# Optimization experiments

Measured on AMD Instinct MI355X. Metric: run time of the kernel, lower is better.

Reference implementation:

```python
import jax, jax.numpy as jnp
import numpy as np

C, A, K, S = 128, 64, 24, 4           # molecules, atoms, neighbors, species
RCR, RCA = 5.2, 3.5                   # radial / angular cutoffs (Angstrom)
ETA_R, ETA_A, ZETA = 16.0, 8.0, 32.0
LAYERS = [384, 160, 128, 96, 1]       # per-element MLP
NPAIR = S * (S + 1) // 2              # 10 unordered species pairs

_triu = np.zeros((S, S), np.int32)
_c = 0
for _i in range(S):
    for _j in range(_i, S):
        _triu[_i, _j] = _triu[_j, _i] = _c
        _c += 1
TRIU = jnp.asarray(_triu)
JJ, KK = np.triu_indices(K, 1)        # static pair-of-neighbors indices, T = K(K-1)/2


def setup_inputs() -> dict:
    key = jax.random.key(0)
    ks = jax.random.split(key, 12)
    element_idxs = jax.random.randint(ks[0], (C, A), 0, S, dtype=jnp.int32)
    neighbor_idxs = jax.random.randint(ks[1], (C, A, K), 0, A, dtype=jnp.int32)
    distances = jax.random.uniform(ks[2], (C, A, K), minval=0.8, maxval=5.0, dtype=jnp.float32)
    dirs = jax.random.normal(ks[3], (C, A, K, 3), dtype=jnp.float32)
    dirs = dirs / jnp.linalg.norm(dirs, axis=-1, keepdims=True)
    diff_vectors = dirs * distances[..., None]
    inp = {"element_idxs": element_idxs, "neighbor_idxs": neighbor_idxs,
           "distances": distances, "diff_vectors": diff_vectors}
    k = 4
    for i, (fin, fout) in enumerate(zip(LAYERS[:-1], LAYERS[1:]), 1):
        inp[f"W{i}"] = jax.random.normal(ks[k], (S, fin, fout), dtype=jnp.float32) / np.sqrt(fin).astype(np.float32); k += 1
        inp[f"b{i}"] = jax.random.normal(ks[k], (S, fout), dtype=jnp.float32) * 0.01; k += 1
    return inp


def _fc(d, rc):
    # smooth cosine cutoff, exactly zero beyond rc
    return jnp.where(d < rc, 0.5 * jnp.cos(np.float32(np.pi) * d / rc) + 0.5, 0.0)


def _celu(x, a=0.1):
    return jnp.where(x > 0, x, a * jnp.expm1(x / a))


def reference(element_idxs, neighbor_idxs, distances, diff_vectors,
              W1, b1, W2, b2, W3, b3, W4, b4):
    shfr = jnp.linspace(0.9, RCR, 17, dtype=jnp.float32)[:-1]                 # (16,)
    shfa = jnp.linspace(0.9, RCA, 5, dtype=jnp.float32)[:-1]                  # (4,)
    shfz = (jnp.arange(8, dtype=jnp.float32) + 0.5) * np.float32(np.pi / 8)   # (8,)

    # species of each neighbor: (C,A,K)
    nspec = element_idxs[jnp.arange(C)[:, None, None], neighbor_idxs]

    # ---- radial sub-AEV: (C,A,S,16) ----
    fcr = _fc(distances, RCR)
    rterm = 0.25 * jnp.exp(-ETA_R * (distances[..., None] - shfr) ** 2) * fcr[..., None]  # (C,A,K,16)
    oh_s = jax.nn.one_hot(nspec, S, dtype=rterm.dtype)                                     # (C,A,K,S)
    radial = jnp.einsum('cakr,caks->casr', rterm, oh_s).reshape(C, A, S * 16)

    # ---- angular sub-AEV over neighbor pairs (j<k): T = K(K-1)/2 ----
    d1, d2 = distances[..., JJ], distances[..., KK]                 # (C,A,T)
    v1, v2 = diff_vectors[..., JJ, :], diff_vectors[..., KK, :]      # (C,A,T,3)
    cosang = jnp.sum(v1 * v2, axis=-1) / (d1 * d2)
    ang = jnp.arccos(0.95 * cosang)                                  # torchani's 0.95 nan-guard
    f1 = ((1.0 + jnp.cos(ang[..., None] - shfz)) * 0.5) ** ZETA      # (C,A,T,8)
    f2 = jnp.exp(-ETA_A * ((d1 + d2) * 0.5)[..., None] - shfa * 0.0) if False else \
         jnp.exp(-ETA_A * (((d1 + d2) * 0.5)[..., None] - shfa) ** 2)  # (C,A,T,4)
    fc12 = _fc(d1, RCA) * _fc(d2, RCA)                               # (C,A,T)
    aterm = (2.0 * f1[..., :, None] * f2[..., None, :] * fc12[..., None, None]).reshape(C, A, JJ.size, 32)
    pidx = TRIU[nspec[..., JJ], nspec[..., KK]]                      # (C,A,T) in [0,10)
    oh_p = jax.nn.one_hot(pidx, NPAIR, dtype=aterm.dtype)            # (C,A,T,10)
    angular = jnp.einsum('catf,catp->capf', aterm, oh_p).reshape(C, A, NPAIR * 32)

    aev = jnp.concatenate([radial, angular], axis=-1)                # (C,A,384)

    # ---- per-element MLPs (computed for all species, then gathered) ----
    h = _celu(jnp.einsum('caf,sfo->caso', aev, W1) + b1)
    h = _celu(jnp.einsum('casf,sfo->caso', h, W2) + b2)
    h = _celu(jnp.einsum('casf,sfo->caso', h, W3) + b3)
    out = (jnp.einsum('casf,sfo->caso', h, W4) + b4)[..., 0]         # (C,A,S)
    atomic = jnp.take_along_axis(out, element_idxs[..., None], axis=2)[..., 0]  # (C,A)
    return atomic.sum(axis=-1)                                       # (C,) molecular energies
```

## Files before the change

kernel.cpp:

```cpp
#include <hip/hip_runtime.h>
#include <math.h>

constexpr int C_ = 128, A_ = 64, K_ = 24, S_ = 4;
constexpr int NATOM = C_ * A_;
constexpr int FAEV = 384;
constexpr float RCR = 5.2f, RCA = 3.5f;
constexpr float PI_F = 3.14159265358979323846f;
constexpr float K_A2 = -8.0f  * 1.44269504f;
constexpr float K_R2 = -64.0f * 1.44269504f;
constexpr float SQRT095 = 0.974679434f;
constexpr float SQRT2   = 1.41421356237f;

constexpr int MLP_TILES = 288;

__global__ __launch_bounds__(256) void aev_kernel(const int* __restrict__ element_idxs,
                                                  const int* __restrict__ neighbor_idxs,
                                                  const float* __restrict__ distances,
                                                  const float* __restrict__ diff_vectors,
                                                  float* __restrict__ aev_out,
                                                  int* __restrict__ mol_cnt,
                                                  int* __restrict__ mol_lst,
                                                  float* __restrict__ out) {
    const int blk = blockIdx.x;
    const int c   = blk >> 4;
    const int t   = threadIdx.x;

    __shared__ int    elem_s[A_];
    __shared__ float4 u4_s[4][K_];
    __shared__ float  fcr_s[4][K_];
    __shared__ float  fca_s[4][K_];
    __shared__ int    spec_s[4][K_];
    __shared__ int    bidx_s[4][S_][K_];
    __shared__ int    nsp_s[4][S_];

    if (t < A_) elem_s[t] = element_idxs[c * A_ + t];
    __syncthreads();

    if ((blk & 15) == 0) {
        if (t < S_) {
            int n = 0;
            int* lst = mol_lst + (c * S_ + t) * A_;
            for (int a = 0; a < A_; ++a)
                if (elem_s[a] == t) lst[n++] = a;
            mol_cnt[c * S_ + t] = n;
        } else if (t == S_) {
            out[c] = 0.0f;
        }
    }

    if (t < 4 * K_) {
        int m = t / K_, k = t - m * K_;
        int base = (blk * 4 + m) * K_ + k;
        int nb = neighbor_idxs[base];
        float d = distances[base];
        float inv = __builtin_amdgcn_rcpf(d) * SQRT095;
        float4 u;
        u.x = diff_vectors[base * 3 + 0] * inv;
        u.y = diff_vectors[base * 3 + 1] * inv;
        u.z = diff_vectors[base * 3 + 2] * inv;
        u.w = 0.5f * d;
        u4_s[m][k] = u;
        spec_s[m][k] = elem_s[nb];
        fcr_s[m][k] = (d < RCR) ? (0.5f * __cosf(PI_F * d * (1.0f / RCR)) + 0.5f) : 0.0f;
        fca_s[m][k] = (d < RCA) ? (SQRT2 * (0.5f * __cosf(PI_F * d * (1.0f / RCA)) + 0.5f)) : 0.0f;
    }
    __syncthreads();

    if (t < 4 * S_) {
        int m = t >> 2, sp = t & 3, n = 0;
        #pragma unroll
        for (int k = 0; k < K_; ++k)
            if (fca_s[m][k] > 0.0f && spec_s[m][k] == sp) bidx_s[m][sp][n++] = k;
        nsp_s[m][sp] = n;
    }
    __syncthreads();

    const int m      = t >> 6;
    const int lane   = t & 63;
    const int lane32 = lane & 31;
    const int par    = lane >> 5;
    float* aev = aev_out + (size_t)(blk * 4 + m) * FAEV;

    {
        const int   spg   = lane >> 4;
        const float shfrh = 0.5f * (0.9f + 0.26875f * (float)(lane & 15));
        float acc = 0.0f;
        #pragma unroll
        for (int k = 0; k < K_; ++k) {
            float hd = u4_s[m][k].w;
            float df = hd - shfrh;
            float term = 0.25f * exp2f(df * df * K_R2) * fcr_s[m][k];
            if (spec_s[m][k] == spg) acc += term;
        }
        aev[lane] = acc;
    }

    const int zz = lane32 >> 2, yy = lane32 & 3;
    const float cz2 = 0.5f * __cosf(((float)zz + 0.5f) * (PI_F / 8.0f));
    const float sz2 = 0.5f * __sinf(((float)zz + 0.5f) * (PI_F / 8.0f));
    const float shfa_l = 0.9f + 0.65f * (float)yy;

    auto pair_term = [&](int j, int k2) -> float {
        float4 u1 = u4_s[m][j], u2 = u4_s[m][k2];
        float ca = u1.x * u2.x + u1.y * u2.y + u1.z * u2.z;
        float sa = sqrtf(1.0f - ca * ca);
        float dd = (u1.w + u2.w) - shfa_l;
        float f2 = exp2f(dd * dd * K_A2);
        float x  = 0.5f + ca * cz2 + sa * sz2;
        float x2 = x * x, x4 = x2 * x2, x8 = x4 * x4, x16 = x8 * x8;
        float tc = fca_s[m][j] * fca_s[m][k2];
        return (x16 * x16) * (f2 * tc);
    };

    #pragma unroll
    for (int spa = 0; spa < 4; ++spa) {
        #pragma unroll
        for (int spb = spa; spb < 4; ++spb) {
            const int pidx = spa * (9 - spa) / 2 + (spb - spa);
            const int na  = nsp_s[m][spa];
            const int nb2 = nsp_s[m][spb];
            float acc = 0.0f;
            if (spa == spb) {
                int jj = 0, kk = 1 + par;
                while (jj < na - 1 && kk >= na) { int ov = kk - na; ++jj; kk = jj + 1 + ov; }
                while (jj < na - 1) {
                    acc += pair_term(bidx_s[m][spa][jj], bidx_s[m][spa][kk]);
                    kk += 2;
                    while (jj < na - 1 && kk >= na) { int ov = kk - na; ++jj; kk = jj + 1 + ov; }
                }
            } else {
                int jj = 0, kk = par;
                while (jj < na && kk >= nb2) { kk -= nb2; ++jj; }
                while (jj < na) {
                    acc += pair_term(bidx_s[m][spa][jj], bidx_s[m][spb][kk]);
                    kk += 2;
                    while (jj < na && kk >= nb2) { kk -= nb2; ++jj; }
                }
            }
            float other = __shfl(acc, lane32 + 32);
            if (lane < 32) aev[64 + pidx * 32 + lane32] = acc + other;
        }
    }
}

__global__ __launch_bounds__(256) void mlp_kernel(const float* __restrict__ aev_ws,
                                                  const int* __restrict__ mol_cnt,
                                                  const int* __restrict__ mol_lst,
                                                  const float* __restrict__ W1, const float* __restrict__ b1,
                                                  const float* __restrict__ W2, const float* __restrict__ b2,
                                                  const float* __restrict__ W3, const float* __restrict__ b3,
                                                  const float* __restrict__ W4, const float* __restrict__ b4,
                                                  float* __restrict__ out) {
    const int blk   = blockIdx.x;
    const int s     = blk & 3;
    const int tile0 = blk >> 2;
    const int t     = threadIdx.x;
    const int lane  = t & 63;

    const int c0 = lane * 2, c1 = c0 + 1;
    const int n0 = mol_cnt[c0 * S_ + s];
    const int n1 = mol_cnt[c1 * S_ + s];
    const int pairc = n0 + n1;
    int scan = pairc;
    #pragma unroll
    for (int off = 1; off < 64; off <<= 1) {
        int v = __shfl_up(scan, off);
        if (lane >= off) scan += v;
    }
    const int cntS = __shfl(scan, 63);

    __shared__ __attribute__((aligned(16))) float aev_s[8][FAEV];
    __shared__ __attribute__((aligned(16))) float h1_s[8][160];
    float (*h2_s)[128] = (float(*)[128])&aev_s[0][0];
    float (*h3_s)[96]  = (float(*)[96])(&aev_s[0][0] + 8 * 128);

    const float* W1s = W1 + s * (FAEV * 160);
    const float* b1s = b1 + s * 160;
    const float* W2s = W2 + s * (160 * 128);
    const float* b2s = b2 + s * 128;
    const float* W3s = W3 + s * (128 * 96);
    const float* b3s = b3 + s * 96;
    const float* W4s = W4 + s * 96;
    const float  bb4 = b4[s];

    for (int tile = tile0; tile * 8 < cntS; tile += MLP_TILES) {
        const int base = tile * 8;

        int myAtom = -1;
        #pragma unroll
        for (int m = 0; m < 8; ++m) {
            int g = base + m;
            int atomAbs = -1;
            if (g < cntS) {
                unsigned long long mask = __ballot(scan > g);
                int L = (int)__builtin_ctzll(mask);
                int exclL = __shfl(scan, L) - __shfl(pairc, L);
                int n0L   = __shfl(n0, L);
                int loc = g - exclL;
                int cL  = 2 * L;
                if (loc >= n0L) { cL += 1; loc -= n0L; }
                atomAbs = cL * A_ + mol_lst[(cL * S_ + s) * A_ + loc];
            }
            if ((t >> 5) == m) myAtom = atomAbs;
        }

        {
            int mrow = t >> 5, l = t & 31;
            float4* dst = (float4*)&aev_s[mrow][0];
            if (myAtom >= 0) {
                const float4* src = (const float4*)(aev_ws + (size_t)myAtom * FAEV);
                dst[l]      = src[l];
                dst[l + 32] = src[l + 32];
                dst[l + 64] = src[l + 64];
            } else {
                dst[l]      = make_float4(0.f, 0.f, 0.f, 0.f);
                dst[l + 32] = make_float4(0.f, 0.f, 0.f, 0.f);
                dst[l + 64] = make_float4(0.f, 0.f, 0.f, 0.f);
            }
        }
        __syncthreads();

        if (t < 160) {
            const float* Wp = W1s + t;
            float acc[8];
            #pragma unroll
            for (int m = 0; m < 8; ++m) acc[m] = 0.0f;
            float wa[4], wb[4];
            #pragma unroll
            for (int j = 0; j < 4; ++j) wa[j] = Wp[j * 160];
            for (int f = 0; f < FAEV; f += 8) {
                const int fb = f + 4;
                #pragma unroll
                for (int j = 0; j < 4; ++j) wb[j] = Wp[(fb + j) * 160];
                #pragma unroll
                for (int m = 0; m < 8; ++m) {
                    float4 av = *(const float4*)&aev_s[m][f];
                    acc[m] += av.x * wa[0] + av.y * wa[1] + av.z * wa[2] + av.w * wa[3];
                }
                const int fa = (f + 8 < FAEV) ? f + 8 : 0;
                #pragma unroll
                for (int j = 0; j < 4; ++j) wa[j] = Wp[(fa + j) * 160];
                #pragma unroll
                for (int m = 0; m < 8; ++m) {
                    float4 av = *(const float4*)&aev_s[m][fb];
                    acc[m] += av.x * wb[0] + av.y * wb[1] + av.z * wb[2] + av.w * wb[3];
                }
            }
            float bb = b1s[t];
            #pragma unroll
            for (int m = 0; m < 8; ++m) {
                float x = acc[m] + bb;
                h1_s[m][t] = (x > 0.f) ? x : 0.1f * (__expf(10.f * x) - 1.f);
            }
        }
        __syncthreads();

        if (t < 128) {
            const float* Wp = W2s + t;
            float acc[8];
            #pragma unroll
            for (int m = 0; m < 8; ++m) acc[m] = 0.0f;
            float wa[4], wb[4];
            #pragma unroll
            for (int j = 0; j < 4; ++j) wa[j] = Wp[j * 128];
            for (int f = 0; f < 160; f += 8) {
                const int fb = f + 4;
                #pragma unroll
                for (int j = 0; j < 4; ++j) wb[j] = Wp[(fb + j) * 128];
                #pragma unroll
                for (int m = 0; m < 8; ++m) {
                    float4 av = *(const float4*)&h1_s[m][f];
                    acc[m] += av.x * wa[0] + av.y * wa[1] + av.z * wa[2] + av.w * wa[3];
                }
                const int fa = (f + 8 < 160) ? f + 8 : 0;
                #pragma unroll
                for (int j = 0; j < 4; ++j) wa[j] = Wp[(fa + j) * 128];
                #pragma unroll
                for (int m = 0; m < 8; ++m) {
                    float4 av = *(const float4*)&h1_s[m][fb];
                    acc[m] += av.x * wb[0] + av.y * wb[1] + av.z * wb[2] + av.w * wb[3];
                }
            }
            float bb = b2s[t];
            #pragma unroll
            for (int m = 0; m < 8; ++m) {
                float x = acc[m] + bb;
                h2_s[m][t] = (x > 0.f) ? x : 0.1f * (__expf(10.f * x) - 1.f);
            }
        }
        __syncthreads();

        if (t < 96) {
            const float* Wp = W3s + t;
            float acc[8];
            #pragma unroll
            for (int m = 0; m < 8; ++m) acc[m] = 0.0f;
            float wa[4], wb[4];
            #pragma unroll
            for (int j = 0; j < 4; ++j) wa[j] = Wp[j * 96];
            for (int f = 0; f < 128; f += 8) {
                const int fb = f + 4;
                #pragma unroll
                for (int j = 0; j < 4; ++j) wb[j] = Wp[(fb + j) * 96];
                #pragma unroll
                for (int m = 0; m < 8; ++m) {
                    float4 av = *(const float4*)&h2_s[m][f];
                    acc[m] += av.x * wa[0] + av.y * wa[1] + av.z * wa[2] + av.w * wa[3];
                }
                const int fa = (f + 8 < 128) ? f + 8 : 0;
                #pragma unroll
                for (int j = 0; j < 4; ++j) wa[j] = Wp[(fa + j) * 96];
                #pragma unroll
                for (int m = 0; m < 8; ++m) {
                    float4 av = *(const float4*)&h2_s[m][fb];
                    acc[m] += av.x * wb[0] + av.y * wb[1] + av.z * wb[2] + av.w * wb[3];
                }
            }
            float bb = b3s[t];
            #pragma unroll
            for (int m = 0; m < 8; ++m) {
                float x = acc[m] + bb;
                h3_s[m][t] = (x > 0.f) ? x : 0.1f * (__expf(10.f * x) - 1.f);
            }
        }
        __syncthreads();

        {
            int m = t >> 5, l = t & 31;
            if (myAtom >= 0) {
                float p = h3_s[m][l]      * W4s[l]
                        + h3_s[m][l + 32] * W4s[l + 32]
                        + h3_s[m][l + 64] * W4s[l + 64];
                #pragma unroll
                for (int off = 16; off >= 1; off >>= 1)
                    p += __shfl_xor(p, off, 32);
                if (l == 0) atomicAdd(&out[myAtom >> 6], p + bb4);
            }
        }
        __syncthreads();
    }
}

extern "C" void kernel_launch(void* const* d_in, const int* in_sizes, int n_in,
                              void* d_out, int out_size, void* d_ws, size_t ws_size,
                              hipStream_t stream) {
    const int*   element_idxs  = (const int*)d_in[0];
    const int*   neighbor_idxs = (const int*)d_in[1];
    const float* distances     = (const float*)d_in[2];
    const float* diff_vectors  = (const float*)d_in[3];
    const float* W1 = (const float*)d_in[4];
    const float* b1 = (const float*)d_in[5];
    const float* W2 = (const float*)d_in[6];
    const float* b2 = (const float*)d_in[7];
    const float* W3 = (const float*)d_in[8];
    const float* b3 = (const float*)d_in[9];
    const float* W4 = (const float*)d_in[10];
    const float* b4 = (const float*)d_in[11];
    float* out = (float*)d_out;

    float* aev_ws  = (float*)d_ws;
    int*   mol_cnt = (int*)((char*)d_ws + (size_t)NATOM * FAEV * 4);
    int*   mol_lst = mol_cnt + C_ * S_;

    hipLaunchKernelGGL(aev_kernel, dim3(NATOM / 4), dim3(256), 0, stream,
                       element_idxs, neighbor_idxs, distances, diff_vectors,
                       aev_ws, mol_cnt, mol_lst, out);
    hipLaunchKernelGGL(mlp_kernel, dim3(S_ * MLP_TILES), dim3(256), 0, stream,
                       aev_ws, mol_cnt, mol_lst,
                       W1, b1, W2, b2, W3, b3, W4, b4, out);
}
```

Baseline: 251.7 us.

## Fuse AEV computation into per-species MLP kernel with global species atom lists

New measurement: 273.7 us. +8.7%, slower.

```diff
diff --git a/kernel.cpp b/kernel.cpp
--- a/kernel.cpp
+++ b/kernel.cpp
@@ -11,164 +11,60 @@
 constexpr float SQRT095 = 0.974679434f;
 constexpr float SQRT2   = 1.41421356237f;
 
-constexpr int MLP_TILES = 288;
-
-__global__ __launch_bounds__(256) void aev_kernel(const int* __restrict__ element_idxs,
-                                                  const int* __restrict__ neighbor_idxs,
-                                                  const float* __restrict__ distances,
-                                                  const float* __restrict__ diff_vectors,
-                                                  float* __restrict__ aev_out,
-                                                  int* __restrict__ mol_cnt,
-                                                  int* __restrict__ mol_lst,
-                                                  float* __restrict__ out) {
-    const int blk = blockIdx.x;
-    const int c   = blk >> 4;
-    const int t   = threadIdx.x;
-
-    __shared__ int    elem_s[A_];
-    __shared__ float4 u4_s[4][K_];
-    __shared__ float  fcr_s[4][K_];
-    __shared__ float  fca_s[4][K_];
-    __shared__ int    spec_s[4][K_];
-    __shared__ int    bidx_s[4][S_][K_];
-    __shared__ int    nsp_s[4][S_];
-
-    if (t < A_) elem_s[t] = element_idxs[c * A_ + t];
+__global__ __launch_bounds__(1024) void setup_kernel(const int* __restrict__ elem,
+                                                     int* __restrict__ cnt,
+                                                     int* __restrict__ glist,
+                                                     float* __restrict__ out) {
+    __shared__ int cnt_s[S_];
+    const int t = threadIdx.x;
+    const int lane = t & 63;
+    if (t < S_) cnt_s[t] = 0;
+    if (t < C_) out[t] = 0.0f;
     __syncthreads();
-
-    if ((blk & 15) == 0) {
-        if (t < S_) {
-            int n = 0;
-            int* lst = mol_lst + (c * S_ + t) * A_;
-            for (int a = 0; a < A_; ++a)
-                if (elem_s[a] == t) lst[n++] = a;
-            mol_cnt[c * S_ + t] = n;
-        } else if (t == S_) {
-            out[c] = 0.0f;
-        }
-    }
-
-    if (t < 4 * K_) {
-        int m = t / K_, k = t - m * K_;
-        int base = (blk * 4 + m) * K_ + k;
-        int nb = neighbor_idxs[base];
-        float d = distances[base];
-        float inv = __builtin_amdgcn_rcpf(d) * SQRT095;
-        float4 u;
-        u.x = diff_vectors[base * 3 + 0] * inv;
-        u.y = diff_vectors[base * 3 + 1] * inv;
-        u.z = diff_vectors[base * 3 + 2] * inv;
-        u.w = 0.5f * d;
-        u4_s[m][k] = u;
-        spec_s[m][k] = elem_s[nb];
-        fcr_s[m][k] = (d < RCR) ? (0.5f * __cosf(PI_F * d * (1.0f / RCR)) + 0.5f) : 0.0f;
-        fca_s[m][k] = (d < RCA) ? (SQRT2 * (0.5f * __cosf(PI_F * d * (1.0f / RCA)) + 0.5f)) : 0.0f;
+    for (int a = t; a < NATOM; a += 1024) {
+        int sp = elem[a];
+        unsigned long long lt = (lane == 0) ? 0ULL : ((~0ULL) >> (64 - lane));
+        int pos = 0;
+        #pragma unroll
+        for (int q = 0; q < S_; ++q) {
+            unsigned long long m = __ballot(sp == q);
+            int cw = (int)__popcll(m);
+            int b = 0;
+            if (lane == 0 && cw) b = atomicAdd(&cnt_s[q], cw);
+            b = __shfl(b, 0);
+            if (sp == q) pos = b + (int)__popcll(m & lt);
+        }
+        glist[sp * NATOM + pos] = a;
     }
     __syncthreads();
-
-    if (t < 4 * S_) {
-        int m = t >> 2, sp = t & 3, n = 0;
-        #pragma unroll
-        for (int k = 0; k < K_; ++k)
-            if (fca_s[m][k] > 0.0f && spec_s[m][k] == sp) bidx_s[m][sp][n++] = k;
-        nsp_s[m][sp] = n;
-    }
-    __syncthreads();
-
-    const int m      = t >> 6;
-    const int lane   = t & 63;
-    const int lane32 = lane & 31;
-    const int par    = lane >> 5;
-    float* aev = aev_out + (size_t)(blk * 4 + m) * FAEV;
-
-    {
-        const int   spg   = lane >> 4;
-        const float shfrh = 0.5f * (0.9f + 0.26875f * (float)(lane & 15));
-        float acc = 0.0f;
-        #pragma unroll
-        for (int k = 0; k < K_; ++k) {
-            float hd = u4_s[m][k].w;
-            float df = hd - shfrh;
-            float term = 0.25f * exp2f(df * df * K_R2) * fcr_s[m][k];
-            if (spec_s[m][k] == spg) acc += term;
-        }
-        aev[lane] = acc;
-    }
-
-    const int zz = lane32 >> 2, yy = lane32 & 3;
-    const float cz2 = 0.5f * __cosf(((float)zz + 0.5f) * (PI_F / 8.0f));
-    const float sz2 = 0.5f * __sinf(((float)zz + 0.5f) * (PI_F / 8.0f));
-    const float shfa_l = 0.9f + 0.65f * (float)yy;
-
-    auto pair_term = [&](int j, int k2) -> float {
-        float4 u1 = u4_s[m][j], u2 = u4_s[m][k2];
-        float ca = u1.x * u2.x + u1.y * u2.y + u1.z * u2.z;
-        float sa = sqrtf(1.0f - ca * ca);
-        float dd = (u1.w + u2.w) - shfa_l;
-        float f2 = exp2f(dd * dd * K_A2);
-        float x  = 0.5f + ca * cz2 + sa * sz2;
-        float x2 = x * x, x4 = x2 * x2, x8 = x4 * x4, x16 = x8 * x8;
-        float tc = fca_s[m][j] * fca_s[m][k2];
-        return (x16 * x16) * (f2 * tc);
-    };
-
-    #pragma unroll
-    for (int spa = 0; spa < 4; ++spa) {
-        #pragma unroll
-        for (int spb = spa; spb < 4; ++spb) {
-            const int pidx = spa * (9 - spa) / 2 + (spb - spa);
-            const int na  = nsp_s[m][spa];
-            const int nb2 = nsp_s[m][spb];
-            float acc = 0.0f;
-            if (spa == spb) {
-                int jj = 0, kk = 1 + par;
-                while (jj < na - 1 && kk >= na) { int ov = kk - na; ++jj; kk = jj + 1 + ov; }
-                while (jj < na - 1) {
-                    acc += pair_term(bidx_s[m][spa][jj], bidx_s[m][spa][kk]);
-                    kk += 2;
-                    while (jj < na - 1 && kk >= na) { int ov = kk - na; ++jj; kk = jj + 1 + ov; }
-                }
-            } else {
-                int jj = 0, kk = par;
-                while (jj < na && kk >= nb2) { kk -= nb2; ++jj; }
-                while (jj < na) {
-                    acc += pair_term(bidx_s[m][spa][jj], bidx_s[m][spb][kk]);
-                    kk += 2;
-                    while (jj < na && kk >= nb2) { kk -= nb2; ++jj; }
-                }
-            }
-            float other = __shfl(acc, lane32 + 32);
-            if (lane < 32) aev[64 + pidx * 32 + lane32] = acc + other;
-        }
-    }
+    if (t < S_) cnt[t] = cnt_s[t];
 }
 
-__global__ __launch_bounds__(256) void mlp_kernel(const float* __restrict__ aev_ws,
-                                                  const int* __restrict__ mol_cnt,
-                                                  const int* __restrict__ mol_lst,
-                                                  const float* __restrict__ W1, const float* __restrict__ b1,
-                                                  const float* __restrict__ W2, const float* __restrict__ b2,
-                                                  const float* __restrict__ W3, const float* __restrict__ b3,
-                                                  const float* __restrict__ W4, const float* __restrict__ b4,
-                                                  float* __restrict__ out) {
-    const int blk   = blockIdx.x;
-    const int s     = blk & 3;
-    const int tile0 = blk >> 2;
+__global__ __launch_bounds__(512, 8) void fused_kernel(const int* __restrict__ elem,
+                                                       const int* __restrict__ nbr,
+                                                       const float* __restrict__ dist,
+                                                       const float* __restrict__ dv,
+                                                       const int* __restrict__ cnt,
+                                                       const int* __restrict__ glist,
+                                                       const float* __restrict__ W1, const float* __restrict__ b1,
+                                                       const float* __restrict__ W2, const float* __restrict__ b2,
+                                                       const float* __restrict__ W3, const float* __restrict__ b3,
+                                                       const float* __restrict__ W4, const float* __restrict__ b4,
+                                                       float* __restrict__ out) {
+    const int s     = blockIdx.x >> 8;
+    const int tile0 = blockIdx.x & 255;
     const int t     = threadIdx.x;
+    const int w     = t >> 6;
     const int lane  = t & 63;
-
-    const int c0 = lane * 2, c1 = c0 + 1;
-    const int n0 = mol_cnt[c0 * S_ + s];
-    const int n1 = mol_cnt[c1 * S_ + s];
-    const int pairc = n0 + n1;
-    int scan = pairc;
-    #pragma unroll
-    for (int off = 1; off < 64; off <<= 1) {
-        int v = __shfl_up(scan, off);
-        if (lane >= off) scan += v;
-    }
-    const int cntS = __shfl(scan, 63);
-
+    const int cntS  = cnt[s];
+
+    __shared__ float4        u4_s[8][K_];
+    __shared__ float         fcr_s[8][K_];
+    __shared__ float         fca_s[8][K_];
+    __shared__ int           spec_s[8][K_];
+    __shared__ unsigned char bidx_s[8][S_][K_];
+    __shared__ int           nsp_s[8][S_];
+    __shared__ int           atom_sh[8];
     __shared__ __attribute__((aligned(16))) float aev_s[8][FAEV];
     __shared__ __attribute__((aligned(16))) float h1_s[8][160];
     float (*h2_s)[128] = (float(*)[128])&aev_s[0][0];
@@ -183,48 +79,109 @@
     const float* W4s = W4 + s * 96;
     const float  bb4 = b4[s];
 
-    for (int tile = tile0; tile * 8 < cntS; tile += MLP_TILES) {
-        const int base = tile * 8;
-
-        int myAtom = -1;
-        #pragma unroll
-        for (int m = 0; m < 8; ++m) {
-            int g = base + m;
-            int atomAbs = -1;
-            if (g < cntS) {
-                unsigned long long mask = __ballot(scan > g);
-                int L = (int)__builtin_ctzll(mask);
-                int exclL = __shfl(scan, L) - __shfl(pairc, L);
-                int n0L   = __shfl(n0, L);
-                int loc = g - exclL;
-                int cL  = 2 * L;
-                if (loc >= n0L) { cL += 1; loc -= n0L; }
-                atomAbs = cL * A_ + mol_lst[(cL * S_ + s) * A_ + loc];
-            }
-            if ((t >> 5) == m) myAtom = atomAbs;
-        }
-
-        {
-            int mrow = t >> 5, l = t & 31;
-            float4* dst = (float4*)&aev_s[mrow][0];
-            if (myAtom >= 0) {
-                const float4* src = (const float4*)(aev_ws + (size_t)myAtom * FAEV);
-                dst[l]      = src[l];
-                dst[l + 32] = src[l + 32];
-                dst[l + 64] = src[l + 64];
-            } else {
-                dst[l]      = make_float4(0.f, 0.f, 0.f, 0.f);
-                dst[l + 32] = make_float4(0.f, 0.f, 0.f, 0.f);
-                dst[l + 64] = make_float4(0.f, 0.f, 0.f, 0.f);
-            }
-        }
-        __syncthreads();
-
-        if (t < 160) {
-            const float* Wp = W1s + t;
-            float acc[8];
-            #pragma unroll
-            for (int m = 0; m < 8; ++m) acc[m] = 0.0f;
+    const int lane32 = lane & 31;
+    const int par    = lane >> 5;
+    const int zz = lane32 >> 2, yy = lane32 & 3;
+    const float cz2 = 0.5f * __cosf(((float)zz + 0.5f) * (PI_F / 8.0f));
+    const float sz2 = 0.5f * __sinf(((float)zz + 0.5f) * (PI_F / 8.0f));
+    const float shfa_l = 0.9f + 0.65f * (float)yy;
+
+    for (int tile = tile0; tile * 8 < cntS; tile += 256) {
+        const int g = tile * 8 + w;
+        const int atomAbs = (g < cntS) ? glist[s * NATOM + g] : -1;
+        if (lane == 0) atom_sh[w] = atomAbs;
+
+        if (atomAbs >= 0 && lane < K_) {
+            int base = atomAbs * K_ + lane;
+            int c    = atomAbs >> 6;
+            int nb   = nbr[base];
+            float d  = dist[base];
+            float inv = __builtin_amdgcn_rcpf(d) * SQRT095;
+            float4 u;
+            u.x = dv[base * 3 + 0] * inv;
+            u.y = dv[base * 3 + 1] * inv;
+            u.z = dv[base * 3 + 2] * inv;
+            u.w = 0.5f * d;
+            u4_s[w][lane]  = u;
+            spec_s[w][lane] = elem[(c << 6) + nb];
+            fcr_s[w][lane] = (d < RCR) ? (0.5f * __cosf(PI_F * d * (1.0f / RCR)) + 0.5f) : 0.0f;
+            fca_s[w][lane] = (d < RCA) ? (SQRT2 * (0.5f * __cosf(PI_F * d * (1.0f / RCA)) + 0.5f)) : 0.0f;
+        }
+        __syncthreads();
+
+        if (atomAbs >= 0 && lane < S_) {
+            int n = 0;
+            #pragma unroll
+            for (int k = 0; k < K_; ++k)
+                if (fca_s[w][k] > 0.0f && spec_s[w][k] == lane)
+                    bidx_s[w][lane][n++] = (unsigned char)k;
+            nsp_s[w][lane] = n;
+        }
+        __syncthreads();
+
+        if (atomAbs >= 0) {
+            {
+                const int   spg   = lane >> 4;
+                const float shfrh = 0.5f * (0.9f + 0.26875f * (float)(lane & 15));
+                float acc = 0.0f;
+                #pragma unroll
+                for (int k = 0; k < K_; ++k) {
+                    float hd = u4_s[w][k].w;
+                    float df = hd - shfrh;
+                    float term = 0.25f * exp2f(df * df * K_R2) * fcr_s[w][k];
+                    if (spec_s[w][k] == spg) acc += term;
+                }
+                aev_s[w][lane] = acc;
+            }
+            auto pair_term = [&](int j, int k2) -> float {
+                float4 u1 = u4_s[w][j], u2 = u4_s[w][k2];
+                float ca = u1.x * u2.x + u1.y * u2.y + u1.z * u2.z;
+                float sa = sqrtf(1.0f - ca * ca);
+                float dd = (u1.w + u2.w) - shfa_l;
+                float f2 = exp2f(dd * dd * K_A2);
+                float x  = 0.5f + ca * cz2 + sa * sz2;
+                float x2 = x * x, x4 = x2 * x2, x8 = x4 * x4, x16 = x8 * x8;
+                float tc = fca_s[w][j] * fca_s[w][k2];
+                return (x16 * x16) * (f2 * tc);
+            };
+            #pragma unroll
+            for (int spa = 0; spa < 4; ++spa) {
+                #pragma unroll
+                for (int spb = spa; spb < 4; ++spb) {
+                    const int pidx = spa * (9 - spa) / 2 + (spb - spa);
+                    const int na  = nsp_s[w][spa];
+                    const int nb2 = nsp_s[w][spb];
+                    float acc = 0.0f;
+                    if (spa == spb) {
+                        int jj = 0, kk = 1 + par;
+                        while (jj < na - 1 && kk >= na) { int ov = kk - na; ++jj; kk = jj + 1 + ov; }
+                        while (jj < na - 1) {
+                            acc += pair_term((int)bidx_s[w][spa][jj], (int)bidx_s[w][spa][kk]);
+                            kk += 2;
+                            while (jj < na - 1 && kk >= na) { int ov = kk - na; ++jj; kk = jj + 1 + ov; }
+                        }
+                    } else {
+                        int jj = 0, kk = par;
+                        while (jj < na && kk >= nb2) { kk -= nb2; ++jj; }
+                        while (jj < na) {
+                            acc += pair_term((int)bidx_s[w][spa][jj], (int)bidx_s[w][spb][kk]);
+                            kk += 2;
+                            while (jj < na && kk >= nb2) { kk -= nb2; ++jj; }
+                        }
+                    }
+                    float other = __shfl(acc, lane32 + 32);
+                    if (lane < 32) aev_s[w][64 + pidx * 32 + lane32] = acc + other;
+                }
+            }
+        }
+        __syncthreads();
+
+        if (t < 320) {
+            const int h  = (t >= 160) ? 1 : 0;
+            const int o  = t - h * 160;
+            const int mb = h * 4;
+            const float* Wp = W1s + o;
+            float acc[4] = {0.f, 0.f, 0.f, 0.f};
             float wa[4], wb[4];
             #pragma unroll
             for (int j = 0; j < 4; ++j) wa[j] = Wp[j * 160];
@@ -233,33 +190,34 @@
                 #pragma unroll
                 for (int j = 0; j < 4; ++j) wb[j] = Wp[(fb + j) * 160];
                 #pragma unroll
-                for (int m = 0; m < 8; ++m) {
-                    float4 av = *(const float4*)&aev_s[m][f];
+                for (int m = 0; m < 4; ++m) {
+                    float4 av = *(const float4*)&aev_s[mb + m][f];
                     acc[m] += av.x * wa[0] + av.y * wa[1] + av.z * wa[2] + av.w * wa[3];
                 }
                 const int fa = (f + 8 < FAEV) ? f + 8 : 0;
                 #pragma unroll
                 for (int j = 0; j < 4; ++j) wa[j] = Wp[(fa + j) * 160];
                 #pragma unroll
-                for (int m = 0; m < 8; ++m) {
-                    float4 av = *(const float4*)&aev_s[m][fb];
+                for (int m = 0; m < 4; ++m) {
+                    float4 av = *(const float4*)&aev_s[mb + m][fb];
                     acc[m] += av.x * wb[0] + av.y * wb[1] + av.z * wb[2] + av.w * wb[3];
                 }
             }
-            float bb = b1s[t];
-            #pragma unroll
-            for (int m = 0; m < 8; ++m) {
+            float bb = b1s[o];
+            #pragma unroll
+            for (int m = 0; m < 4; ++m) {
                 float x = acc[m] + bb;
-                h1_s[m][t] = (x > 0.f) ? x : 0.1f * (__expf(10.f * x) - 1.f);
-            }
-        }
-        __syncthreads();
-
-        if (t < 128) {
-            const float* Wp = W2s + t;
-            float acc[8];
-            #pragma unroll
-            for (int m = 0; m < 8; ++m) acc[m] = 0.0f;
+                h1_s[mb + m][o] = (x > 0.f) ? x : 0.1f * (__expf(10.f * x) - 1.f);
+            }
+        }
+        __syncthreads();
+
+        if (t < 256) {
+            const int h  = t >> 7;
+            const int o  = t & 127;
+            const int mb = h * 4;
+            const float* Wp = W2s + o;
+            float acc[4] = {0.f, 0.f, 0.f, 0.f};
             float wa[4], wb[4];
             #pragma unroll
             for (int j = 0; j < 4; ++j) wa[j] = Wp[j * 128];
@@ -268,33 +226,34 @@
                 #pragma unroll
                 for (int j = 0; j < 4; ++j) wb[j] = Wp[(fb + j) * 128];
                 #pragma unroll
-                for (int m = 0; m < 8; ++m) {
-                    float4 av = *(const float4*)&h1_s[m][f];
+                for (int m = 0; m < 4; ++m) {
+                    float4 av = *(const float4*)&h1_s[mb + m][f];
                     acc[m] += av.x * wa[0] + av.y * wa[1] + av.z * wa[2] + av.w * wa[3];
                 }
                 const int fa = (f + 8 < 160) ? f + 8 : 0;
                 #pragma unroll
                 for (int j = 0; j < 4; ++j) wa[j] = Wp[(fa + j) * 128];
                 #pragma unroll
-                for (int m = 0; m < 8; ++m) {
-                    float4 av = *(const float4*)&h1_s[m][fb];
+                for (int m = 0; m < 4; ++m) {
+                    float4 av = *(const float4*)&h1_s[mb + m][fb];
                     acc[m] += av.x * wb[0] + av.y * wb[1] + av.z * wb[2] + av.w * wb[3];
                 }
             }
-            float bb = b2s[t];
-            #pragma unroll
-            for (int m = 0; m < 8; ++m) {
+            float bb = b2s[o];
+            #pragma unroll
+            for (int m = 0; m < 4; ++m) {
                 float x = acc[m] + bb;
-                h2_s[m][t] = (x > 0.f) ? x : 0.1f * (__expf(10.f * x) - 1.f);
-            }
-        }
-        __syncthreads();
-
-        if (t < 96) {
-            const float* Wp = W3s + t;
-            float acc[8];
-            #pragma unroll
-            for (int m = 0; m < 8; ++m) acc[m] = 0.0f;
+                h2_s[mb + m][o] = (x > 0.f) ? x : 0.1f * (__expf(10.f * x) - 1.f);
+            }
+        }
+        __syncthreads();
+
+        if (t < 192) {
+            const int h  = (t >= 96) ? 1 : 0;
+            const int o  = t - h * 96;
+            const int mb = h * 4;
+            const float* Wp = W3s + o;
+            float acc[4] = {0.f, 0.f, 0.f, 0.f};
             float wa[4], wb[4];
             #pragma unroll
             for (int j = 0; j < 4; ++j) wa[j] = Wp[j * 96];
@@ -303,38 +262,39 @@
                 #pragma unroll
                 for (int j = 0; j < 4; ++j) wb[j] = Wp[(fb + j) * 96];
                 #pragma unroll
-                for (int m = 0; m < 8; ++m) {
-                    float4 av = *(const float4*)&h2_s[m][f];
+                for (int m = 0; m < 4; ++m) {
+                    float4 av = *(const float4*)&h2_s[mb + m][f];
                     acc[m] += av.x * wa[0] + av.y * wa[1] + av.z * wa[2] + av.w * wa[3];
                 }
                 const int fa = (f + 8 < 128) ? f + 8 : 0;
                 #pragma unroll
                 for (int j = 0; j < 4; ++j) wa[j] = Wp[(fa + j) * 96];
                 #pragma unroll
-                for (int m = 0; m < 8; ++m) {
-                    float4 av = *(const float4*)&h2_s[m][fb];
+                for (int m = 0; m < 4; ++m) {
+                    float4 av = *(const float4*)&h2_s[mb + m][fb];
                     acc[m] += av.x * wb[0] + av.y * wb[1] + av.z * wb[2] + av.w * wb[3];
                 }
             }
-            float bb = b3s[t];
-            #pragma unroll
-            for (int m = 0; m < 8; ++m) {
+            float bb = b3s[o];
+            #pragma unroll
+            for (int m = 0; m < 4; ++m) {
                 float x = acc[m] + bb;
-                h3_s[m][t] = (x > 0.f) ? x : 0.1f * (__expf(10.f * x) - 1.f);
-            }
-        }
-        __syncthreads();
-
-        {
+                h3_s[mb + m][o] = (x > 0.f) ? x : 0.1f * (__expf(10.f * x) - 1.f);
+            }
+        }
+        __syncthreads();
+
+        if (t < 256) {
             int m = t >> 5, l = t & 31;
-            if (myAtom >= 0) {
+            int a = atom_sh[m];
+            if (a >= 0) {
                 float p = h3_s[m][l]      * W4s[l]
                         + h3_s[m][l + 32] * W4s[l + 32]
                         + h3_s[m][l + 64] * W4s[l + 64];
                 #pragma unroll
                 for (int off = 16; off >= 1; off >>= 1)
                     p += __shfl_xor(p, off, 32);
-                if (l == 0) atomicAdd(&out[myAtom >> 6], p + bb4);
+                if (l == 0) atomicAdd(&out[a >> 6], p + bb4);
             }
         }
         __syncthreads();
@@ -358,14 +318,13 @@
     const float* b4 = (const float*)d_in[11];
     float* out = (float*)d_out;
 
-    float* aev_ws  = (float*)d_ws;
-    int*   mol_cnt = (int*)((char*)d_ws + (size_t)NATOM * FAEV * 4);
-    int*   mol_lst = mol_cnt + C_ * S_;
-
-    hipLaunchKernelGGL(aev_kernel, dim3(NATOM / 4), dim3(256), 0, stream,
+    int* cnt   = (int*)d_ws;
+    int* glist = cnt + 4;
+
+    hipLaunchKernelGGL(setup_kernel, dim3(1), dim3(1024), 0, stream,
+                       element_idxs, cnt, glist, out);
+    hipLaunchKernelGGL(fused_kernel, dim3(S_ * 256), dim3(512), 0, stream,
                        element_idxs, neighbor_idxs, distances, diff_vectors,
-                       aev_ws, mol_cnt, mol_lst, out);
-    hipLaunchKernelGGL(mlp_kernel, dim3(S_ * MLP_TILES), dim3(256), 0, stream,
-                       aev_ws, mol_cnt, mol_lst,
+                       cnt, glist,
                        W1, b1, W2, b2, W3, b3, W4, b4, out);
 }
```
